# Kernel optimization log

Hardware: AMD Instinct MI355X
Metric: run time of the kernel (lower is better)

Reference implementation:

```python
import jax, jax.numpy as jnp
import numpy as np

RES = 128
RADIUS = 1.3
SH_DEG = 2
SH_DIM = (SH_DEG + 1) ** 2            # 9
DATA_DIM = SH_DIM * 3 + 1             # 28
VOXEL = RADIUS * 2.0 / RES
STEP = VOXEL / 2.0
N_SAMPLES = int(np.ceil(np.sqrt(3.0) * 2 * RES))  # 444


def sh_basis(d):
    # real spherical harmonics basis, degree 2 (9 coeffs); d: [B,3]
    d = d / (jnp.linalg.norm(d, axis=-1, keepdims=True) + 1e-9)
    x, y, z = d[..., 0], d[..., 1], d[..., 2]
    C0 = 0.28209479177387814
    C1 = 0.4886025119029199
    C20, C21, C22, C23, C24 = (1.0925484305920792, -1.0925484305920792,
                               0.31539156525252005, -1.0925484305920792,
                               0.5462742152960396)
    return jnp.stack([
        jnp.full_like(x, C0),
        -C1 * y, C1 * z, -C1 * x,
        C20 * x * y, C21 * y * z,
        C22 * (2.0 * z * z - x * x - y * y),
        C23 * x * z, C24 * (x * x - y * y),
    ], axis=-1)  # [B, 9]


def trilinear(data, pts):
    # data: [C, D, H, W]; pts: [N, 3] (x,y,z) in [-1,1]; align_corners=True
    # matches torch grid_sample convention: x indexes W, y indexes H, z indexes D
    R = data.shape[-1]
    g = jnp.clip((pts + 1.0) * 0.5 * (R - 1), 0.0, R - 1)
    i0 = jnp.clip(jnp.floor(g).astype(jnp.int32), 0, R - 2)
    f = g - i0.astype(g.dtype)
    x0, y0, z0 = i0[:, 0], i0[:, 1], i0[:, 2]
    fx, fy, fz = f[:, 0], f[:, 1], f[:, 2]
    def gat(dz, dy, dx):
        return data[:, z0 + dz, y0 + dy, x0 + dx]  # [C, N]
    wx0, wx1 = 1.0 - fx, fx
    wy0, wy1 = 1.0 - fy, fy
    wz0, wz1 = 1.0 - fz, fz
    return (gat(0, 0, 0) * (wz0 * wy0 * wx0) + gat(0, 0, 1) * (wz0 * wy0 * wx1)
          + gat(0, 1, 0) * (wz0 * wy1 * wx0) + gat(0, 1, 1) * (wz0 * wy1 * wx1)
          + gat(1, 0, 0) * (wz1 * wy0 * wx0) + gat(1, 0, 1) * (wz1 * wy0 * wx1)
          + gat(1, 1, 0) * (wz1 * wy1 * wx0) + gat(1, 1, 1) * (wz1 * wy1 * wx1))


def setup_inputs() -> dict:
    key = jax.random.key(0)
    k1, k2, k3 = jax.random.split(key, 3)
    B = 4096
    rays_o = 0.3 * jax.random.normal(k1, (B, 3), dtype=jnp.float32)
    rays_d = jax.random.normal(k2, (B, 3), dtype=jnp.float32)
    # grid init as in module (0.1 for SH, 0.01 for sigma) plus small noise
    base = jnp.concatenate([
        jnp.full((DATA_DIM - 1, RES, RES, RES), 0.1, dtype=jnp.float32),
        jnp.full((1, RES, RES, RES), 0.01, dtype=jnp.float32)], axis=0)
    data = base + 0.01 * jax.random.normal(k3, (DATA_DIM, RES, RES, RES), dtype=jnp.float32)
    return {"rays_o": rays_o, "rays_d": rays_d, "data": data}


def reference(rays_o, rays_d, data):
    B = rays_o.shape[0]
    # ray-AABB intersection with cube [-RADIUS, RADIUS]^3
    inv_d = 1.0 / rays_d
    t0 = (-RADIUS - rays_o) * inv_d
    t1 = (RADIUS - rays_o) * inv_d
    tmin = jnp.maximum(jnp.max(jnp.minimum(t0, t1), axis=-1), 0.0)  # [B]
    tmax = jnp.min(jnp.maximum(t0, t1), axis=-1)                    # [B]
    offsets = jnp.arange(N_SAMPLES + 1, dtype=rays_o.dtype) * STEP
    intersections = tmin[:, None] + offsets[None, :]                # [B, N+1]
    t_mid = intersections[:, :-1]                                   # [B, N]
    pts = rays_o[:, None, :] + rays_d[:, None, :] * t_mid[..., None]  # [B,N,3]
    inside = jnp.all(jnp.abs(pts) <= RADIUS, axis=-1)
    mask = inside & (t_mid < tmax[:, None]) & (tmin[:, None] < tmax[:, None])
    pts_n = pts / RADIUS                                            # normalize_coord
    interp = trilinear(data, pts_n.reshape(-1, 3)).T                # [B*N, C]
    interp = interp.reshape(B, N_SAMPLES, DATA_DIM)
    # masked scatter == dense interp zeroed where mask is False
    sigma = jax.nn.relu(jnp.where(mask, interp[..., -1], 0.0))      # [B, N]
    dists = (intersections[:, 1:] - intersections[:, :-1]) * jnp.linalg.norm(rays_d, axis=-1, keepdims=True)
    alpha = 1.0 - jnp.exp(-sigma * dists)                           # [B, N]
    Tcum = jnp.cumprod(1.0 - alpha + 1e-10, axis=-1)
    Tshift = jnp.concatenate([jnp.ones_like(Tcum[:, :1]), Tcum[:, :-1]], axis=-1)
    abs_light = alpha * Tshift                                      # [B, N]
    sh_mult = sh_basis(rays_d)                                      # [B, 9]
    sh = interp[..., :-1].reshape(B, N_SAMPLES, 3, SH_DIM)
    rgb = jnp.einsum('bnck,bk->bnc', sh, sh_mult)                   # [B,N,3]
    rgb = jax.nn.sigmoid(jnp.where(mask[..., None], rgb, 0.0))
    out = jnp.sum(abs_light[..., None] * rgb, axis=1)               # [B, 3]
    acc = jnp.sum(abs_light, axis=-1, keepdims=True)
    out = out + (1.0 - acc)  # white background
    return out
```

## Files before the change

kernel.cpp:

```cpp
#include <hip/hip_runtime.h>
#include <hip/hip_fp16.h>

#define RESG 128
#define NVOX (RESG * RESG * RESG)
#define NCH 28
#define NSAMP 444
#define NCHUNK 7

typedef float f32x2 __attribute__((ext_vector_type(2)));

#if __has_builtin(__builtin_amdgcn_cvt_scalef32_pk_f32_fp4)
#define HW_DEC4 1
#else
#define HW_DEC4 0
#endif

static __device__ __forceinline__ float dec_nib(unsigned int n) {
    const unsigned int em = n & 7u;
    float mag;
    if (em < 2u) {
        mag = 0.5f * (float)em;
    } else {
        union { unsigned int u; float f; } c;
        c.u = (((em >> 1) + 126u) << 23) | ((em & 1u) << 22);
        mag = c.f;
    }
    return (n & 8u) ? -mag : mag;
}
template <int SEL>
static __device__ __forceinline__ f32x2 dec4(unsigned int dw) {
#if HW_DEC4
    return __builtin_amdgcn_cvt_scalef32_pk_f32_fp4(dw, 1.0f, SEL);
#else
    const unsigned int b = (dw >> (8 * SEL)) & 0xFFu;
    f32x2 r;
    r.x = dec_nib(b & 15u);
    r.y = dec_nib(b >> 4);
    return r;
#endif
}
static __device__ __forceinline__ unsigned int enc_nib(float f) {
    const unsigned int s = (__float_as_uint(f) >> 28) & 8u;
    const float a = fabsf(f);
    unsigned int em;
    if (a < 1.75f) em = (unsigned int)__float2int_rn(a * 2.0f);
    else if (a < 2.5f) em = 4u;
    else if (a < 3.5f) em = 5u;
    else if (a < 5.0f) em = 6u;
    else em = 7u;
    return s | em;
}
static __device__ __forceinline__ unsigned int enc_pair(float a, float b) {
    return enc_nib(a) | (enc_nib(b) << 4);
}

static __device__ __forceinline__ void enc_voxel(const float* __restrict__ s,
                                                 unsigned int* __restrict__ d) {
#pragma unroll
    for (int j = 0; j < 3; ++j) {
        d[j] = enc_pair(s[8 * j + 0] * 32.0f, s[8 * j + 1] * 32.0f) |
               (enc_pair(s[8 * j + 2] * 32.0f, s[8 * j + 3] * 32.0f) << 8) |
               (enc_pair(s[8 * j + 4] * 32.0f, s[8 * j + 5] * 32.0f) << 16) |
               (enc_pair(s[8 * j + 6] * 32.0f, s[8 * j + 7] * 32.0f) << 24);
    }
    union { __half h; unsigned short u; } sg;
    sg.h = __float2half(s[27]);
    d[3] = enc_pair(s[24] * 32.0f, s[25] * 32.0f) |
           (enc_pair(s[26] * 32.0f, 0.0f) << 8) | ((unsigned int)sg.u << 16);
}

__global__ __launch_bounds__(256) void pack4x2_k(const float* __restrict__ src,
                                                 uint4* __restrict__ dst) {
    const int t = blockIdx.x * 256 + threadIdx.x;
    float a[NCH], b[NCH];
#pragma unroll
    for (int c = 0; c < NCH; ++c) {
        const float2 s2 = reinterpret_cast<const float2*>(src + (size_t)c * NVOX)[t];
        a[c] = s2.x;
        b[c] = s2.y;
    }
    unsigned int da[4], db[4];
    enc_voxel(a, da);
    enc_voxel(b, db);
    dst[2 * (size_t)t] = make_uint4(da[0], da[1], da[2], da[3]);
    dst[2 * (size_t)t + 1] = make_uint4(db[0], db[1], db[2], db[3]);
}

__global__ __launch_bounds__(128) void render4_k(const float* __restrict__ ro,
                                                 const float* __restrict__ rd,
                                                 const uint4* __restrict__ gb,
                                                 float* __restrict__ out, int B) {
    const int ray = blockIdx.x;
    if (ray >= B) return;
    const int wid = (int)(threadIdx.x >> 6);
    const int lane = (int)(threadIdx.x & 63);

    __shared__ float sres[NCHUNK][5];
    if (threadIdx.x < NCHUNK) {
        sres[threadIdx.x][0] = 0.0f;
        sres[threadIdx.x][1] = 0.0f;
        sres[threadIdx.x][2] = 0.0f;
        sres[threadIdx.x][3] = 0.0f;
        sres[threadIdx.x][4] = 1.0f;
    }
    __syncthreads();

    const float RAD = 1.3f;
    const float STEPF = (float)(1.3 * 2.0 / 128.0 / 2.0);

    const float ox = ro[ray * 3 + 0], oy = ro[ray * 3 + 1], oz = ro[ray * 3 + 2];
    const float dxr = rd[ray * 3 + 0], dyr = rd[ray * 3 + 1], dzr = rd[ray * 3 + 2];

    const float ivx = 1.0f / dxr, ivy = 1.0f / dyr, ivz = 1.0f / dzr;
    const float t0x = (-RAD - ox) * ivx, t1x = (RAD - ox) * ivx;
    const float t0y = (-RAD - oy) * ivy, t1y = (RAD - oy) * ivy;
    const float t0z = (-RAD - oz) * ivz, t1z = (RAD - oz) * ivz;
    float tmin = fmaxf(fmaxf(fminf(t0x, t1x), fminf(t0y, t1y)), fminf(t0z, t1z));
    tmin = fmaxf(tmin, 0.0f);
    const float tmax = fminf(fminf(fmaxf(t0x, t1x), fmaxf(t0y, t1y)), fmaxf(t0z, t1z));

    const float nrm = sqrtf(dxr * dxr + dyr * dyr + dzr * dzr);
    const float dist = STEPF * nrm;

    const float inn = 1.0f / (nrm + 1e-9f);
    const float x = dxr * inn, y = dyr * inn, z = dzr * inn;
    float sh[9];
    sh[0] = 0.28209479177387814f;
    sh[1] = -0.4886025119029199f * y;
    sh[2] = 0.4886025119029199f * z;
    sh[3] = -0.4886025119029199f * x;
    sh[4] = 1.0925484305920792f * x * y;
    sh[5] = -1.0925484305920792f * y * z;
    sh[6] = 0.31539156525252005f * (2.0f * z * z - x * x - y * y);
    sh[7] = -1.0925484305920792f * x * z;
    sh[8] = 0.5462742152960396f * (x * x - y * y);

    if (tmin < tmax) {
        for (int c = wid; c < NCHUNK; c += 2) {
            const float tb = tmin + (float)(c * 64) * STEPF;
            if (tb >= tmax) break;

            const int sidx = c * 64 + lane;
            const float t = tmin + (float)sidx * STEPF;
            const float px = ox + dxr * t, py = oy + dyr * t, pz = oz + dzr * t;
            const bool live = (sidx < NSAMP) && (t < tmax) && (fabsf(px) <= RAD) &&
                              (fabsf(py) <= RAD) && (fabsf(pz) <= RAD);
            float alpha = 0.f, cr = 0.f, cg = 0.f, cb = 0.f;
            if (live) {
                float gx = fminf(fmaxf((px / RAD + 1.0f) * 0.5f * 127.0f, 0.0f), 127.0f);
                float gy = fminf(fmaxf((py / RAD + 1.0f) * 0.5f * 127.0f, 0.0f), 127.0f);
                float gz = fminf(fmaxf((pz / RAD + 1.0f) * 0.5f * 127.0f, 0.0f), 127.0f);
                const int x0 = min((int)gx, 126);
                const int y0 = min((int)gy, 126);
                const int z0 = min((int)gz, 126);
                const float fx = gx - (float)x0;
                const float fy = gy - (float)y0;
                const float fz = gz - (float)z0;

                float wc[8];
#pragma unroll
                for (int c8 = 0; c8 < 8; ++c8) {
                    wc[c8] = ((c8 & 4) ? fz : 1.0f - fz) * ((c8 & 2) ? fy : 1.0f - fy) *
                             ((c8 & 1) ? fx : 1.0f - fx);
                }

                const unsigned int cell = (unsigned int)((z0 * RESG + y0) * RESG + x0);
                float f[NCH];
#pragma unroll
                for (int cc = 0; cc < NCH; ++cc) f[cc] = 0.0f;
#pragma unroll
                for (int g = 0; g < 2; ++g) {
                    uint4 q[4];
#pragma unroll
                    for (int k = 0; k < 4; ++k) {
                        const int c8 = g * 4 + k;
                        const unsigned int vi = cell + ((c8 >> 2) & 1) * (RESG * RESG) +
                                                ((c8 >> 1) & 1) * RESG + (c8 & 1);
                        q[k] = gb[(size_t)vi];
                    }
#pragma unroll
                    for (int k = 0; k < 4; ++k) {
                        const float w = wc[g * 4 + k];
                        const float ws = w * 0.03125f;
                        f32x2 p;
                        p = dec4<0>(q[k].x); f[0] += ws * p.x;  f[1] += ws * p.y;
                        p = dec4<1>(q[k].x); f[2] += ws * p.x;  f[3] += ws * p.y;
                        p = dec4<2>(q[k].x); f[4] += ws * p.x;  f[5] += ws * p.y;
                        p = dec4<3>(q[k].x); f[6] += ws * p.x;  f[7] += ws * p.y;
                        p = dec4<0>(q[k].y); f[8] += ws * p.x;  f[9] += ws * p.y;
                        p = dec4<1>(q[k].y); f[10] += ws * p.x; f[11] += ws * p.y;
                        p = dec4<2>(q[k].y); f[12] += ws * p.x; f[13] += ws * p.y;
                        p = dec4<3>(q[k].y); f[14] += ws * p.x; f[15] += ws * p.y;
                        p = dec4<0>(q[k].z); f[16] += ws * p.x; f[17] += ws * p.y;
                        p = dec4<1>(q[k].z); f[18] += ws * p.x; f[19] += ws * p.y;
                        p = dec4<2>(q[k].z); f[20] += ws * p.x; f[21] += ws * p.y;
                        p = dec4<3>(q[k].z); f[22] += ws * p.x; f[23] += ws * p.y;
                        p = dec4<0>(q[k].w); f[24] += ws * p.x; f[25] += ws * p.y;
                        p = dec4<1>(q[k].w); f[26] += ws * p.x;
                        union { unsigned short u; __half h; } sg;
                        sg.u = (unsigned short)(q[k].w >> 16);
                        f[27] += w * __half2float(sg.h);
                    }
                }
                const float sigma = fmaxf(f[27], 0.0f);
                float r = 0.f, g = 0.f, b = 0.f;
#pragma unroll
                for (int k = 0; k < 9; ++k) {
                    r += sh[k] * f[k];
                    g += sh[k] * f[9 + k];
                    b += sh[k] * f[18 + k];
                }
                alpha = 1.0f - __expf(-sigma * dist);
                cr = 1.0f / (1.0f + __expf(-r));
                cg = 1.0f / (1.0f + __expf(-g));
                cb = 1.0f / (1.0f + __expf(-b));
            }
            const float wfac = 1.0f - alpha + 1e-10f;
            float incl = wfac;
#pragma unroll
            for (int off = 1; off < 64; off <<= 1) {
                const float u = __shfl_up(incl, off);
                if (lane >= off) incl *= u;
            }
            float excl = __shfl_up(incl, 1);
            if (lane == 0) excl = 1.0f;
            const float al = alpha * excl;
            float pR = al * cr, pG = al * cg, pB = al * cb, pA = al;
#pragma unroll
            for (int off = 32; off; off >>= 1) {
                pR += __shfl_xor(pR, off);
                pG += __shfl_xor(pG, off);
                pB += __shfl_xor(pB, off);
                pA += __shfl_xor(pA, off);
            }
            const float Pc = __shfl(incl, 63);
            if (lane == 0) {
                sres[c][0] = pR;
                sres[c][1] = pG;
                sres[c][2] = pB;
                sres[c][3] = pA;
                sres[c][4] = Pc;
            }
        }
    }
    __syncthreads();
    if (threadIdx.x == 0) {
        float T = 1.0f, R = 0.f, G = 0.f, Bl = 0.f, A = 0.f;
#pragma unroll
        for (int c = 0; c < NCHUNK; ++c) {
            R += T * sres[c][0];
            G += T * sres[c][1];
            Bl += T * sres[c][2];
            A += T * sres[c][3];
            T *= sres[c][4];
        }
        const float bg = 1.0f - A;
        out[ray * 3 + 0] = R + bg;
        out[ray * 3 + 1] = G + bg;
        out[ray * 3 + 2] = Bl + bg;
    }
}

__global__ __launch_bounds__(128) void render_f32_k(const float* __restrict__ ro,
                                                    const float* __restrict__ rd,
                                                    const float* __restrict__ gf,
                                                    float* __restrict__ out, int B) {
    const int ray = blockIdx.x;
    if (ray >= B) return;
    const int wid = (int)(threadIdx.x >> 6);
    const int lane = (int)(threadIdx.x & 63);

    __shared__ float sres[NCHUNK][5];
    if (threadIdx.x < NCHUNK) {
        sres[threadIdx.x][0] = 0.0f;
        sres[threadIdx.x][1] = 0.0f;
        sres[threadIdx.x][2] = 0.0f;
        sres[threadIdx.x][3] = 0.0f;
        sres[threadIdx.x][4] = 1.0f;
    }
    __syncthreads();

    const float RAD = 1.3f;
    const float STEPF = (float)(1.3 * 2.0 / 128.0 / 2.0);
    const float ox = ro[ray * 3 + 0], oy = ro[ray * 3 + 1], oz = ro[ray * 3 + 2];
    const float dxr = rd[ray * 3 + 0], dyr = rd[ray * 3 + 1], dzr = rd[ray * 3 + 2];
    const float ivx = 1.0f / dxr, ivy = 1.0f / dyr, ivz = 1.0f / dzr;
    const float t0x = (-RAD - ox) * ivx, t1x = (RAD - ox) * ivx;
    const float t0y = (-RAD - oy) * ivy, t1y = (RAD - oy) * ivy;
    const float t0z = (-RAD - oz) * ivz, t1z = (RAD - oz) * ivz;
    float tmin = fmaxf(fmaxf(fminf(t0x, t1x), fminf(t0y, t1y)), fminf(t0z, t1z));
    tmin = fmaxf(tmin, 0.0f);
    const float tmax = fminf(fminf(fmaxf(t0x, t1x), fmaxf(t0y, t1y)), fmaxf(t0z, t1z));
    const float nrm = sqrtf(dxr * dxr + dyr * dyr + dzr * dzr);
    const float dist = STEPF * nrm;
    const float inn = 1.0f / (nrm + 1e-9f);
    const float x = dxr * inn, y = dyr * inn, z = dzr * inn;
    float sh[9];
    sh[0] = 0.28209479177387814f;
    sh[1] = -0.4886025119029199f * y;
    sh[2] = 0.4886025119029199f * z;
    sh[3] = -0.4886025119029199f * x;
    sh[4] = 1.0925484305920792f * x * y;
    sh[5] = -1.0925484305920792f * y * z;
    sh[6] = 0.31539156525252005f * (2.0f * z * z - x * x - y * y);
    sh[7] = -1.0925484305920792f * x * z;
    sh[8] = 0.5462742152960396f * (x * x - y * y);

    if (tmin < tmax) {
        for (int c = wid; c < NCHUNK; c += 2) {
            const float tb = tmin + (float)(c * 64) * STEPF;
            if (tb >= tmax) break;
            const int sidx = c * 64 + lane;
            const float t = tmin + (float)sidx * STEPF;
            const float px = ox + dxr * t, py = oy + dyr * t, pz = oz + dzr * t;
            const bool live = (sidx < NSAMP) && (t < tmax) && (fabsf(px) <= RAD) &&
                              (fabsf(py) <= RAD) && (fabsf(pz) <= RAD);
            float alpha = 0.f, cr = 0.f, cg = 0.f, cb = 0.f;
            if (live) {
                float gx = fminf(fmaxf((px / RAD + 1.0f) * 0.5f * 127.0f, 0.0f), 127.0f);
                float gy = fminf(fmaxf((py / RAD + 1.0f) * 0.5f * 127.0f, 0.0f), 127.0f);
                float gz = fminf(fmaxf((pz / RAD + 1.0f) * 0.5f * 127.0f, 0.0f), 127.0f);
                const int x0 = min((int)gx, 126);
                const int y0 = min((int)gy, 126);
                const int z0 = min((int)gz, 126);
                const float fx = gx - (float)x0;
                const float fy = gy - (float)y0;
                const float fz = gz - (float)z0;
                float f[NCH];
#pragma unroll
                for (int cc = 0; cc < NCH; ++cc) f[cc] = 0.0f;
                const size_t cell = (size_t)(z0 * RESG + y0) * RESG + x0;
#pragma unroll
                for (int c8 = 0; c8 < 8; ++c8) {
                    const float w = ((c8 & 4) ? fz : 1.0f - fz) * ((c8 & 2) ? fy : 1.0f - fy) *
                                    ((c8 & 1) ? fx : 1.0f - fx);
                    const float* p = gf + cell + ((c8 >> 2) & 1) * (RESG * RESG) +
                                     ((c8 >> 1) & 1) * RESG + (c8 & 1);
#pragma unroll
                    for (int cc = 0; cc < NCH; ++cc) f[cc] += w * p[(size_t)cc * NVOX];
                }
                const float sigma = fmaxf(f[27], 0.0f);
                float r = 0.f, g = 0.f, b = 0.f;
#pragma unroll
                for (int k = 0; k < 9; ++k) {
                    r += sh[k] * f[k];
                    g += sh[k] * f[9 + k];
                    b += sh[k] * f[18 + k];
                }
                alpha = 1.0f - __expf(-sigma * dist);
                cr = 1.0f / (1.0f + __expf(-r));
                cg = 1.0f / (1.0f + __expf(-g));
                cb = 1.0f / (1.0f + __expf(-b));
            }
            float incl = 1.0f - alpha + 1e-10f;
#pragma unroll
            for (int off = 1; off < 64; off <<= 1) {
                const float u = __shfl_up(incl, off);
                if (lane >= off) incl *= u;
            }
            float excl = __shfl_up(incl, 1);
            if (lane == 0) excl = 1.0f;
            const float al = alpha * excl;
            float pR = al * cr, pG = al * cg, pB = al * cb, pA = al;
#pragma unroll
            for (int off = 32; off; off >>= 1) {
                pR += __shfl_xor(pR, off);
                pG += __shfl_xor(pG, off);
                pB += __shfl_xor(pB, off);
                pA += __shfl_xor(pA, off);
            }
            const float Pc = __shfl(incl, 63);
            if (lane == 0) {
                sres[c][0] = pR;
                sres[c][1] = pG;
                sres[c][2] = pB;
                sres[c][3] = pA;
                sres[c][4] = Pc;
            }
        }
    }
    __syncthreads();
    if (threadIdx.x == 0) {
        float T = 1.0f, R = 0.f, G = 0.f, Bl = 0.f, A = 0.f;
#pragma unroll
        for (int c = 0; c < NCHUNK; ++c) {
            R += T * sres[c][0];
            G += T * sres[c][1];
            Bl += T * sres[c][2];
            A += T * sres[c][3];
            T *= sres[c][4];
        }
        const float bg = 1.0f - A;
        out[ray * 3 + 0] = R + bg;
        out[ray * 3 + 1] = G + bg;
        out[ray * 3 + 2] = Bl + bg;
    }
}

extern "C" void kernel_launch(void* const* d_in, const int* in_sizes, int n_in,
                              void* d_out, int out_size, void* d_ws, size_t ws_size,
                              hipStream_t stream) {
    const float* rays_o = (const float*)d_in[0];
    const float* rays_d = (const float*)d_in[1];
    const float* data = (const float*)d_in[2];
    float* out = (float*)d_out;
    const int B = in_sizes[0] / 3;

    const size_t need = (size_t)NVOX * 16;

    if (d_ws != nullptr && ws_size >= need) {
        uint4* gridp = (uint4*)d_ws;
        pack4x2_k<<<NVOX / 2 / 256, 256, 0, stream>>>(data, gridp);
        render4_k<<<B, 128, 0, stream>>>(rays_o, rays_d, gridp, out, B);
    } else {
        render_f32_k<<<B, 128, 0, stream>>>(rays_o, rays_d, data, out, B);
    }
}
```

Before: 86.80 us.

## Bin rays by direction octant and render through a slot table

```diff
diff --git a/kernel.cpp b/kernel.cpp
--- a/kernel.cpp
+++ b/kernel.cpp
@@ -6,6 +6,7 @@
 #define NCH 28
 #define NSAMP 444
 #define NCHUNK 7
+#define SLOTCAP 1024
 
 typedef float f32x2 __attribute__((ext_vector_type(2)));
 
@@ -54,44 +55,55 @@
     return enc_nib(a) | (enc_nib(b) << 4);
 }
 
-static __device__ __forceinline__ void enc_voxel(const float* __restrict__ s,
-                                                 unsigned int* __restrict__ d) {
+__global__ __launch_bounds__(256) void pack4_k(const float* __restrict__ src,
+                                               uint4* __restrict__ dst) {
+    const int v = blockIdx.x * 256 + threadIdx.x;
+    float s[NCH];
+#pragma unroll
+    for (int c = 0; c < NCH; ++c) s[c] = src[(size_t)c * NVOX + v];
+#pragma unroll
+    for (int c = 0; c < 27; ++c) s[c] *= 32.0f;
+    unsigned int d[4];
 #pragma unroll
     for (int j = 0; j < 3; ++j) {
-        d[j] = enc_pair(s[8 * j + 0] * 32.0f, s[8 * j + 1] * 32.0f) |
-               (enc_pair(s[8 * j + 2] * 32.0f, s[8 * j + 3] * 32.0f) << 8) |
-               (enc_pair(s[8 * j + 4] * 32.0f, s[8 * j + 5] * 32.0f) << 16) |
-               (enc_pair(s[8 * j + 6] * 32.0f, s[8 * j + 7] * 32.0f) << 24);
+        d[j] = enc_pair(s[8 * j + 0], s[8 * j + 1]) |
+               (enc_pair(s[8 * j + 2], s[8 * j + 3]) << 8) |
+               (enc_pair(s[8 * j + 4], s[8 * j + 5]) << 16) |
+               (enc_pair(s[8 * j + 6], s[8 * j + 7]) << 24);
     }
     union { __half h; unsigned short u; } sg;
     sg.h = __float2half(s[27]);
-    d[3] = enc_pair(s[24] * 32.0f, s[25] * 32.0f) |
-           (enc_pair(s[26] * 32.0f, 0.0f) << 8) | ((unsigned int)sg.u << 16);
-}
-
-__global__ __launch_bounds__(256) void pack4x2_k(const float* __restrict__ src,
-                                                 uint4* __restrict__ dst) {
-    const int t = blockIdx.x * 256 + threadIdx.x;
-    float a[NCH], b[NCH];
-#pragma unroll
-    for (int c = 0; c < NCH; ++c) {
-        const float2 s2 = reinterpret_cast<const float2*>(src + (size_t)c * NVOX)[t];
-        a[c] = s2.x;
-        b[c] = s2.y;
-    }
-    unsigned int da[4], db[4];
-    enc_voxel(a, da);
-    enc_voxel(b, db);
-    dst[2 * (size_t)t] = make_uint4(da[0], da[1], da[2], da[3]);
-    dst[2 * (size_t)t + 1] = make_uint4(db[0], db[1], db[2], db[3]);
-}
-
-__global__ __launch_bounds__(128) void render4_k(const float* __restrict__ ro,
-                                                 const float* __restrict__ rd,
-                                                 const uint4* __restrict__ gb,
-                                                 float* __restrict__ out, int B) {
-    const int ray = blockIdx.x;
-    if (ray >= B) return;
+    d[3] = enc_pair(s[24], s[25]) | (enc_pair(s[26], 0.0f) << 8) |
+           ((unsigned int)sg.u << 16);
+    dst[(size_t)v] = make_uint4(d[0], d[1], d[2], d[3]);
+}
+
+__global__ __launch_bounds__(256) void init_slots_k(int* __restrict__ slots,
+                                                    int* __restrict__ cnt) {
+    const int gid = blockIdx.x * 256 + threadIdx.x;
+    if (gid < 8 * SLOTCAP) slots[gid] = -1;
+    if (gid < 8) cnt[gid] = 0;
+}
+
+__global__ __launch_bounds__(256) void bin_k(const float* __restrict__ rd,
+                                             int* __restrict__ slots,
+                                             int* __restrict__ cnt, int B) {
+    const int r = blockIdx.x * 256 + threadIdx.x;
+    if (r >= B) return;
+    const int o = ((rd[r * 3 + 0] < 0.0f) ? 1 : 0) | ((rd[r * 3 + 1] < 0.0f) ? 2 : 0) |
+                  ((rd[r * 3 + 2] < 0.0f) ? 4 : 0);
+    const int pos = atomicAdd(&cnt[o], 1);
+    if (pos < SLOTCAP) slots[o * SLOTCAP + pos] = r;
+}
+
+__global__ __launch_bounds__(128) void render4o_k(const float* __restrict__ ro,
+                                                  const float* __restrict__ rd,
+                                                  const uint4* __restrict__ gb,
+                                                  const int* __restrict__ slots,
+                                                  float* __restrict__ out, int B) {
+    const int b = blockIdx.x;
+    const int ray = slots[(b & 7) * SLOTCAP + (b >> 3)];
+    if (ray < 0) return;
     const int wid = (int)(threadIdx.x >> 6);
     const int lane = (int)(threadIdx.x & 63);
 
@@ -203,17 +215,17 @@
                     }
                 }
                 const float sigma = fmaxf(f[27], 0.0f);
-                float r = 0.f, g = 0.f, b = 0.f;
+                float r = 0.f, g = 0.f, b2 = 0.f;
 #pragma unroll
                 for (int k = 0; k < 9; ++k) {
                     r += sh[k] * f[k];
                     g += sh[k] * f[9 + k];
-                    b += sh[k] * f[18 + k];
+                    b2 += sh[k] * f[18 + k];
                 }
                 alpha = 1.0f - __expf(-sigma * dist);
                 cr = 1.0f / (1.0f + __expf(-r));
                 cg = 1.0f / (1.0f + __expf(-g));
-                cb = 1.0f / (1.0f + __expf(-b));
+                cb = 1.0f / (1.0f + __expf(-b2));
             }
             const float wfac = 1.0f - alpha + 1e-10f;
             float incl = wfac;
@@ -406,12 +418,18 @@
     float* out = (float*)d_out;
     const int B = in_sizes[0] / 3;
 
-    const size_t need = (size_t)NVOX * 16;
-
-    if (d_ws != nullptr && ws_size >= need) {
+    const size_t grid_bytes = (size_t)NVOX * 16;
+    const size_t slots_bytes = (size_t)(8 * SLOTCAP + 8) * 4;
+    const size_t need = grid_bytes + slots_bytes;
+
+    if (d_ws != nullptr && ws_size >= need && B <= 8 * SLOTCAP) {
         uint4* gridp = (uint4*)d_ws;
-        pack4x2_k<<<NVOX / 2 / 256, 256, 0, stream>>>(data, gridp);
-        render4_k<<<B, 128, 0, stream>>>(rays_o, rays_d, gridp, out, B);
+        int* slots = (int*)((char*)d_ws + grid_bytes);
+        int* cnt = slots + 8 * SLOTCAP;
+        pack4_k<<<NVOX / 256, 256, 0, stream>>>(data, gridp);
+        init_slots_k<<<(8 * SLOTCAP + 255) / 256, 256, 0, stream>>>(slots, cnt);
+        bin_k<<<(B + 255) / 256, 256, 0, stream>>>(rays_d, slots, cnt, B);
+        render4o_k<<<8 * SLOTCAP, 128, 0, stream>>>(rays_o, rays_d, gridp, slots, out, B);
     } else {
         render_f32_k<<<B, 128, 0, stream>>>(rays_o, rays_d, data, out, B);
     }
```

After: 105.5 us. 21.6% more time.
